# Kernel tuning notes

Measured on AMD Instinct MI355X. Metric: run time of the kernel, lower is better.

## Reference

```python
import jax, jax.numpy as jnp
import numpy as np

N_TOTAL = 204800  # total valid nodes across the batch
B = 1024          # number of graphs
D = 512           # input_dim (dim_node)
H = 512           # hidden width of NonLinearClassifier
C = 52            # num_classes
EPS = 1e-5        # BatchNorm eps


def setup_inputs() -> dict:
    key = jax.random.key(0)
    kz, k1, k2, k3 = jax.random.split(key, 4)
    # ragged per-graph node counts summing exactly to N_TOTAL
    rng = np.random.default_rng(0)
    counts = rng.integers(50, 350, size=B).astype(np.float64)
    counts = np.floor(counts * N_TOTAL / counts.sum()).astype(np.int64)
    counts[-1] += N_TOTAL - counts.sum()
    assert counts.min() > 0 and counts.sum() == N_TOTAL
    return {
        "z": jax.random.normal(kz, (N_TOTAL, D), dtype=jnp.float32),
        "batch_num_nodes": jnp.asarray(counts, dtype=jnp.int64),
        "w1": jax.random.normal(k1, (D, H), dtype=jnp.float32) * 0.02,
        "b1": jnp.zeros((H,), jnp.float32),
        "g1": jnp.ones((H,), jnp.float32),
        "beta1": jnp.zeros((H,), jnp.float32),
        "w2": jax.random.normal(k2, (H, H), dtype=jnp.float32) * 0.02,
        "b2": jnp.zeros((H,), jnp.float32),
        "g2": jnp.ones((H,), jnp.float32),
        "beta2": jnp.zeros((H,), jnp.float32),
        "w3": jax.random.normal(k3, (H, C), dtype=jnp.float32) * 0.02,
        "b3": jnp.zeros((C,), jnp.float32),
    }


def _batchnorm(x, gamma, beta):
    # training-mode BatchNorm1d: batch statistics (biased variance)
    m = x.mean(axis=0)
    v = x.var(axis=0)
    return gamma * (x - m) * jax.lax.rsqrt(v + EPS) + beta


def reference(z, batch_num_nodes, w1, b1, g1, beta1, w2, b2, g2, beta2, w3, b3):
    # fused segment-mean pooling (replaces torch.split + per-graph .mean loop)
    seg_ids = jnp.repeat(jnp.arange(B), batch_num_nodes, total_repeat_length=N_TOTAL)
    sums = jax.ops.segment_sum(z, seg_ids, num_segments=B)          # [B, D]
    graph_feats = sums / batch_num_nodes.astype(z.dtype)[:, None]   # [B, D]
    # NonLinearClassifier MLP (dropout inactive in eval / deterministic ref)
    h = jax.nn.relu(_batchnorm(graph_feats @ w1 + b1, g1, beta1))
    h = jax.nn.relu(_batchnorm(h @ w2 + b2, g2, beta2))
    return h @ w3 + b3  # [B, C] logits
```

## Files before the change

### kernel.cpp

```cpp
#include <hip/hip_runtime.h>

#define N_TOTAL 204800
#define NB 1024
#define DIM 512
#define NC 52
#define BN_EPS 1e-5f

typedef float nf4 __attribute__((ext_vector_type(4)));

__device__ inline float bn_relu1(float v, int f,
                                 const float* __restrict__ s1, const float* __restrict__ s2,
                                 const float* __restrict__ g, const float* __restrict__ beta) {
    float m  = s1[f] * (1.0f / NB);
    float vv = s2[f] * (1.0f / NB) - m * m;
    float is = rsqrtf(vv + BN_EPS);
    float h  = g[f] * (v - m) * is + beta[f];
    return h > 0.f ? h : 0.f;
}

__global__ __launch_bounds__(256) void k_pool(const float* __restrict__ z,
                                              const int* __restrict__ bnn,
                                              float* __restrict__ stats,
                                              float* __restrict__ X) {
    __shared__ nf4 buf[3][32];
    __shared__ int redA[4], redB[4];
    int g   = blockIdx.x;
    int cc  = blockIdx.y;
    int tid = threadIdx.x;
    int lane = tid & 63;
    int w    = tid >> 6;

    int t_all = 0;
#pragma unroll
    for (int k = 0; k < 4; k++) t_all += bnn[tid + k * 256];
#pragma unroll
    for (int s = 1; s < 64; s <<= 1) t_all += __shfl_xor(t_all, s);
    if (lane == 0) redA[w] = t_all;
    __syncthreads();
    bool is64 = (redA[0] + redA[1] + redA[2] + redA[3]) != N_TOTAL;

    int t_pre = 0;
#pragma unroll
    for (int k = 0; k < 4; k++) {
        int j = tid + k * 256;
        if (j < g) t_pre += is64 ? bnn[2 * j] : bnn[j];
    }
#pragma unroll
    for (int s = 1; s < 64; s <<= 1) t_pre += __shfl_xor(t_pre, s);
    if (lane == 0) redB[w] = t_pre;
    if (cc == 0 && g < 8) stats[g * 256 + tid] = 0.0f;
    __syncthreads();
    int s0 = redB[0] + redB[1] + redB[2] + redB[3];
    int n  = is64 ? bnn[2 * g] : bnn[g];
    float r = 1.0f / (float)n;

    int c4 = tid & 31;
    int rp = tid >> 5;
    const nf4* p = (const nf4*)z + (size_t)s0 * 128 + cc * 32 + c4;
    nf4 a0 = {0,0,0,0}, a1 = {0,0,0,0}, a2 = {0,0,0,0}, a3 = {0,0,0,0};
    int i = rp;
    for (; i + 56 < n; i += 64) {
        nf4 v0 = __builtin_nontemporal_load(&p[(size_t)(i +  0) * 128]);
        nf4 v1 = __builtin_nontemporal_load(&p[(size_t)(i +  8) * 128]);
        nf4 v2 = __builtin_nontemporal_load(&p[(size_t)(i + 16) * 128]);
        nf4 v3 = __builtin_nontemporal_load(&p[(size_t)(i + 24) * 128]);
        nf4 v4 = __builtin_nontemporal_load(&p[(size_t)(i + 32) * 128]);
        nf4 v5 = __builtin_nontemporal_load(&p[(size_t)(i + 40) * 128]);
        nf4 v6 = __builtin_nontemporal_load(&p[(size_t)(i + 48) * 128]);
        nf4 v7 = __builtin_nontemporal_load(&p[(size_t)(i + 56) * 128]);
        a0 += v0; a1 += v1; a2 += v2; a3 += v3;
        a0 += v4; a1 += v5; a2 += v6; a3 += v7;
    }
    for (; i < n; i += 8) {
        a0 += __builtin_nontemporal_load(&p[(size_t)i * 128]);
    }
    a0 += a1; a2 += a3; a0 += a2;
    a0.x += __shfl_xor(a0.x, 32); a0.y += __shfl_xor(a0.y, 32);
    a0.z += __shfl_xor(a0.z, 32); a0.w += __shfl_xor(a0.w, 32);
    if (w > 0 && lane < 32) buf[w - 1][c4] = a0;
    __syncthreads();
    if (w == 0 && lane < 32) {
        a0 += buf[0][c4]; a0 += buf[1][c4]; a0 += buf[2][c4];
        a0 *= r;
        ((nf4*)X)[(size_t)g * 128 + cc * 32 + c4] = a0;
    }
}

template <bool BNA>
__global__ __launch_bounds__(512) void k_gemm32x64(const float* __restrict__ A,
                                                   const float* __restrict__ W,
                                                   const float* __restrict__ bias,
                                                   const float* __restrict__ ps1,
                                                   const float* __restrict__ ps2,
                                                   const float* __restrict__ gam,
                                                   const float* __restrict__ bet,
                                                   float* __restrict__ Y,
                                                   float* __restrict__ os1,
                                                   float* __restrict__ os2) {
    __shared__ float As[32][34];
    __shared__ float Ws[32][68];
    int tid = threadIdx.x;
    int tx = tid & 31, ty = tid >> 5;
    int gr0 = blockIdx.x * 32;
    int gc0 = blockIdx.y * 64;

    int arow = (tid & 255) >> 3;
    int akq  = tid & 7;
    int wk  = tid >> 4;
    int wcq = tid & 15;

    float acc[2][2] = {};

    float4 ra = {0, 0, 0, 0};
    if (tid < 256) ra = *(const float4*)&A[(size_t)(gr0 + arow) * DIM + akq * 4];
    float4 rw = *(const float4*)&W[(size_t)wk * DIM + gc0 + wcq * 4];

    for (int kt = 0; kt < 16; kt++) {
        if (tid < 256) {
            float4 v = ra;
            if (BNA) {
                int f0 = kt * 32 + akq * 4;
                v.x = bn_relu1(v.x, f0 + 0, ps1, ps2, gam, bet);
                v.y = bn_relu1(v.y, f0 + 1, ps1, ps2, gam, bet);
                v.z = bn_relu1(v.z, f0 + 2, ps1, ps2, gam, bet);
                v.w = bn_relu1(v.w, f0 + 3, ps1, ps2, gam, bet);
            }
            As[akq * 4 + 0][arow] = v.x;
            As[akq * 4 + 1][arow] = v.y;
            As[akq * 4 + 2][arow] = v.z;
            As[akq * 4 + 3][arow] = v.w;
        }
        *(float4*)&Ws[wk][wcq * 4] = rw;
        __syncthreads();

        if (kt < 15) {
            int k0 = (kt + 1) * 32;
            if (tid < 256)
                ra = *(const float4*)&A[(size_t)(gr0 + arow) * DIM + k0 + akq * 4];
            rw = *(const float4*)&W[(size_t)(k0 + wk) * DIM + gc0 + wcq * 4];
        }

#pragma unroll
        for (int k = 0; k < 32; k++) {
            float2 a = *(const float2*)&As[k][ty * 2];
            float2 w = *(const float2*)&Ws[k][tx * 2];
            acc[0][0] += a.x * w.x; acc[0][1] += a.x * w.y;
            acc[1][0] += a.y * w.x; acc[1][1] += a.y * w.y;
        }
        __syncthreads();
    }

    float2 b = *(const float2*)&bias[gc0 + tx * 2];
    float s0 = 0, s1 = 0, q0 = 0, q1 = 0;
#pragma unroll
    for (int i = 0; i < 2; i++) {
        float2 y;
        y.x = acc[i][0] + b.x;
        y.y = acc[i][1] + b.y;
        *(float2*)&Y[(size_t)(gr0 + ty * 2 + i) * DIM + gc0 + tx * 2] = y;
        s0 += y.x; q0 += y.x * y.x;
        s1 += y.y; q1 += y.y * y.y;
    }
    s0 += __shfl_xor(s0, 32); q0 += __shfl_xor(q0, 32);
    s1 += __shfl_xor(s1, 32); q1 += __shfl_xor(q1, 32);
    if ((tid & 63) < 32) {
        atomicAdd(&os1[gc0 + tx * 2 + 0], s0);
        atomicAdd(&os1[gc0 + tx * 2 + 1], s1);
        atomicAdd(&os2[gc0 + tx * 2 + 0], q0);
        atomicAdd(&os2[gc0 + tx * 2 + 1], q1);
    }
}

__global__ __launch_bounds__(256) void k_gemm3(const float* __restrict__ Y2,
                                               const float* __restrict__ W,
                                               const float* __restrict__ bias,
                                               const float* __restrict__ s1,
                                               const float* __restrict__ s2,
                                               const float* __restrict__ gam,
                                               const float* __restrict__ bet,
                                               float* __restrict__ out) {
    __shared__ float As[4][DIM];
    int tid = threadIdx.x;
    int r0 = blockIdx.x * 4;
#pragma unroll
    for (int it = 0; it < 2; it++) {
        int idx = it * 256 + tid;
        int row = idx >> 7;
        int cq  = idx & 127;
        int f   = cq * 4;
        float4 v = *(const float4*)&Y2[(size_t)(r0 + row) * DIM + f];
        v.x = bn_relu1(v.x, f + 0, s1, s2, gam, bet);
        v.y = bn_relu1(v.y, f + 1, s1, s2, gam, bet);
        v.z = bn_relu1(v.z, f + 2, s1, s2, gam, bet);
        v.w = bn_relu1(v.w, f + 3, s1, s2, gam, bet);
        *(float4*)&As[row][f] = v;
    }
    __syncthreads();
    int col = tid & 63;
    int row = tid >> 6;
    if (col < NC) {
        float acc = 0.f;
#pragma unroll 8
        for (int k = 0; k < DIM; k += 4) {
            float4 a = *(const float4*)&As[row][k];
            acc += a.x * W[(size_t)(k + 0) * NC + col];
            acc += a.y * W[(size_t)(k + 1) * NC + col];
            acc += a.z * W[(size_t)(k + 2) * NC + col];
            acc += a.w * W[(size_t)(k + 3) * NC + col];
        }
        out[(size_t)(r0 + row) * NC + col] = acc + bias[col];
    }
}

extern "C" void kernel_launch(void* const* d_in, const int* in_sizes, int n_in,
                              void* d_out, int out_size, void* d_ws, size_t ws_size,
                              hipStream_t stream) {
    const float* z   = (const float*)d_in[0];
    const int*   bnn = (const int*)d_in[1];
    const float* w1  = (const float*)d_in[2];
    const float* b1  = (const float*)d_in[3];
    const float* g1  = (const float*)d_in[4];
    const float* be1 = (const float*)d_in[5];
    const float* w2  = (const float*)d_in[6];
    const float* b2  = (const float*)d_in[7];
    const float* g2  = (const float*)d_in[8];
    const float* be2 = (const float*)d_in[9];
    const float* w3  = (const float*)d_in[10];
    const float* b3  = (const float*)d_in[11];

    float* stats = (float*)d_ws;
    float* X     = stats + 2048;
    float* Y1    = X  + (size_t)NB * DIM;
    float* Y2    = Y1 + (size_t)NB * DIM;
    float* out   = (float*)d_out;

    k_pool<<<dim3(NB, 4), 256, 0, stream>>>(z, bnn, stats, X);

    dim3 gg(NB / 32, DIM / 64);
    k_gemm32x64<false><<<gg, 512, 0, stream>>>(X, w1, b1,
                                               nullptr, nullptr, nullptr, nullptr,
                                               Y1, stats, stats + 512);
    k_gemm32x64<true><<<gg, 512, 0, stream>>>(Y1, w2, b2,
                                              stats, stats + 512, g1, be1,
                                              Y2, stats + 1024, stats + 1536);
    k_gemm3<<<NB / 4, 256, 0, stream>>>(Y2, w3, b3,
                                        stats + 1024, stats + 1536, g2, be2, out);
}
```

Baseline: 619.9 us.

## Fuse three MLP GEMM kernels into one persistent kernel with grid barriers

Replaces the two GEMM launches and the final classifier launch with a single 256-block kernel that runs all three stages in sequence, separated by a software grid barrier built on atomic counters. Each block now computes a 32x64 tile with 256 threads doing 2x4 outputs apiece, replacing 512 threads doing 2x2. The goal is to remove kernel-launch gaps and tail effects between the small MLP stages. The cost is barrier spin overhead, and correctness depends on all 256 blocks being resident at the same time.

```diff
diff --git a/kernel.cpp b/kernel.cpp
--- a/kernel.cpp
+++ b/kernel.cpp
@@ -21,6 +21,7 @@
 __global__ __launch_bounds__(256) void k_pool(const float* __restrict__ z,
                                               const int* __restrict__ bnn,
                                               float* __restrict__ stats,
+                                              unsigned* __restrict__ bar,
                                               float* __restrict__ X) {
     __shared__ nf4 buf[3][32];
     __shared__ int redA[4], redB[4];
@@ -49,6 +50,7 @@
     for (int s = 1; s < 64; s <<= 1) t_pre += __shfl_xor(t_pre, s);
     if (lane == 0) redB[w] = t_pre;
     if (cc == 0 && g < 8) stats[g * 256 + tid] = 0.0f;
+    if (cc == 0 && g == 8 && tid < 4) bar[tid] = 0u;
     __syncthreads();
     int s0 = redB[0] + redB[1] + redB[2] + redB[3];
     int n  = is64 ? bnn[2 * g] : bnn[g];
@@ -86,102 +88,149 @@
     }
 }
 
+
+__device__ inline void grid_barrier(unsigned* cnt, unsigned* gen) {
+    __threadfence();
+    __syncthreads();
+    if (threadIdx.x == 0) {
+        unsigned g = atomicAdd(gen, 0u);
+        unsigned old = atomicAdd(cnt, 1u);
+        if (old == 255u) {
+            atomicExch(cnt, 0u);
+            atomicAdd(gen, 1u);
+        } else {
+            while (atomicAdd(gen, 0u) == g) { }
+        }
+    }
+    __syncthreads();
+    __threadfence();
+}
+
 template <bool BNA>
-__global__ __launch_bounds__(512) void k_gemm32x64(const float* __restrict__ A,
-                                                   const float* __restrict__ W,
-                                                   const float* __restrict__ bias,
-                                                   const float* __restrict__ ps1,
-                                                   const float* __restrict__ ps2,
-                                                   const float* __restrict__ gam,
-                                                   const float* __restrict__ bet,
-                                                   float* __restrict__ Y,
-                                                   float* __restrict__ os1,
-                                                   float* __restrict__ os2) {
+__device__ void gemm_phase(const float* __restrict__ A,
+                           const float* __restrict__ W,
+                           const float* __restrict__ bias,
+                           const float* __restrict__ ps1,
+                           const float* __restrict__ ps2,
+                           const float* __restrict__ gam,
+                           const float* __restrict__ bet,
+                           float* __restrict__ Y,
+                           float* __restrict__ os1,
+                           float* __restrict__ os2,
+                           float (&As)[32][34], float (&Ws)[32][68]) {
+    int tid = threadIdx.x;
+    int tx = tid & 15, ty = tid >> 4;
+    int gr0 = (blockIdx.x >> 3) * 32;
+    int gc0 = (blockIdx.x & 7) * 64;
+
+    int arow = tid >> 3;
+    int akq  = tid & 7;
+    int wk0 = tid >> 4;
+    int wcq = tid & 15;
+
+    float acc[2][4] = {};
+
+    float4 ra  = *(const float4*)&A[(size_t)(gr0 + arow) * DIM + akq * 4];
+    float4 rw0 = *(const float4*)&W[(size_t)wk0 * DIM + gc0 + wcq * 4];
+    float4 rw1 = *(const float4*)&W[(size_t)(wk0 + 16) * DIM + gc0 + wcq * 4];
+
+    for (int kt = 0; kt < 16; kt++) {
+        float4 v = ra;
+        if (BNA) {
+            int f0 = kt * 32 + akq * 4;
+            v.x = bn_relu1(v.x, f0 + 0, ps1, ps2, gam, bet);
+            v.y = bn_relu1(v.y, f0 + 1, ps1, ps2, gam, bet);
+            v.z = bn_relu1(v.z, f0 + 2, ps1, ps2, gam, bet);
+            v.w = bn_relu1(v.w, f0 + 3, ps1, ps2, gam, bet);
+        }
+        As[akq * 4 + 0][arow] = v.x;
+        As[akq * 4 + 1][arow] = v.y;
+        As[akq * 4 + 2][arow] = v.z;
+        As[akq * 4 + 3][arow] = v.w;
+        *(float4*)&Ws[wk0][wcq * 4]      = rw0;
+        *(float4*)&Ws[wk0 + 16][wcq * 4] = rw1;
+        __syncthreads();
+
+        if (kt < 15) {
+            int k0 = (kt + 1) * 32;
+            ra  = *(const float4*)&A[(size_t)(gr0 + arow) * DIM + k0 + akq * 4];
+            rw0 = *(const float4*)&W[(size_t)(k0 + wk0) * DIM + gc0 + wcq * 4];
+            rw1 = *(const float4*)&W[(size_t)(k0 + wk0 + 16) * DIM + gc0 + wcq * 4];
+        }
+
+#pragma unroll
+        for (int k = 0; k < 32; k++) {
+            float2 a = *(const float2*)&As[k][ty * 2];
+            float4 w = *(const float4*)&Ws[k][tx * 4];
+            acc[0][0] += a.x * w.x; acc[0][1] += a.x * w.y;
+            acc[0][2] += a.x * w.z; acc[0][3] += a.x * w.w;
+            acc[1][0] += a.y * w.x; acc[1][1] += a.y * w.y;
+            acc[1][2] += a.y * w.z; acc[1][3] += a.y * w.w;
+        }
+        __syncthreads();
+    }
+
+    float4 b = *(const float4*)&bias[gc0 + tx * 4];
+    float s[4] = {}, q[4] = {};
+#pragma unroll
+    for (int i = 0; i < 2; i++) {
+        float4 y;
+        y.x = acc[i][0] + b.x;
+        y.y = acc[i][1] + b.y;
+        y.z = acc[i][2] + b.z;
+        y.w = acc[i][3] + b.w;
+        *(float4*)&Y[(size_t)(gr0 + ty * 2 + i) * DIM + gc0 + tx * 4] = y;
+        s[0] += y.x; q[0] += y.x * y.x;
+        s[1] += y.y; q[1] += y.y * y.y;
+        s[2] += y.z; q[2] += y.z * y.z;
+        s[3] += y.w; q[3] += y.w * y.w;
+    }
+#pragma unroll
+    for (int j = 0; j < 4; j++) {
+        s[j] += __shfl_xor(s[j], 16); s[j] += __shfl_xor(s[j], 32);
+        q[j] += __shfl_xor(q[j], 16); q[j] += __shfl_xor(q[j], 32);
+    }
+    if ((ty & 3) == 0) {
+#pragma unroll
+        for (int j = 0; j < 4; j++) {
+            atomicAdd(&os1[gc0 + tx * 4 + j], s[j]);
+            atomicAdd(&os2[gc0 + tx * 4 + j], q[j]);
+        }
+    }
+}
+
+__global__ __launch_bounds__(256) void k_mlp(const float* __restrict__ X,
+                                             const float* __restrict__ w1,
+                                             const float* __restrict__ b1,
+                                             const float* __restrict__ g1,
+                                             const float* __restrict__ be1,
+                                             const float* __restrict__ w2,
+                                             const float* __restrict__ b2,
+                                             const float* __restrict__ g2,
+                                             const float* __restrict__ be2,
+                                             const float* __restrict__ w3,
+                                             const float* __restrict__ b3,
+                                             float* __restrict__ stats,
+                                             unsigned* __restrict__ bar,
+                                             float* __restrict__ Y1,
+                                             float* __restrict__ Y2,
+                                             float* __restrict__ out) {
     __shared__ float As[32][34];
     __shared__ float Ws[32][68];
-    int tid = threadIdx.x;
-    int tx = tid & 31, ty = tid >> 5;
-    int gr0 = blockIdx.x * 32;
-    int gc0 = blockIdx.y * 64;
-
-    int arow = (tid & 255) >> 3;
-    int akq  = tid & 7;
-    int wk  = tid >> 4;
-    int wcq = tid & 15;
-
-    float acc[2][2] = {};
-
-    float4 ra = {0, 0, 0, 0};
-    if (tid < 256) ra = *(const float4*)&A[(size_t)(gr0 + arow) * DIM + akq * 4];
-    float4 rw = *(const float4*)&W[(size_t)wk * DIM + gc0 + wcq * 4];
-
-    for (int kt = 0; kt < 16; kt++) {
-        if (tid < 256) {
-            float4 v = ra;
-            if (BNA) {
-                int f0 = kt * 32 + akq * 4;
-                v.x = bn_relu1(v.x, f0 + 0, ps1, ps2, gam, bet);
-                v.y = bn_relu1(v.y, f0 + 1, ps1, ps2, gam, bet);
-                v.z = bn_relu1(v.z, f0 + 2, ps1, ps2, gam, bet);
-                v.w = bn_relu1(v.w, f0 + 3, ps1, ps2, gam, bet);
-            }
-            As[akq * 4 + 0][arow] = v.x;
-            As[akq * 4 + 1][arow] = v.y;
-            As[akq * 4 + 2][arow] = v.z;
-            As[akq * 4 + 3][arow] = v.w;
-        }
-        *(float4*)&Ws[wk][wcq * 4] = rw;
-        __syncthreads();
-
-        if (kt < 15) {
-            int k0 = (kt + 1) * 32;
-            if (tid < 256)
-                ra = *(const float4*)&A[(size_t)(gr0 + arow) * DIM + k0 + akq * 4];
-            rw = *(const float4*)&W[(size_t)(k0 + wk) * DIM + gc0 + wcq * 4];
-        }
-
-#pragma unroll
-        for (int k = 0; k < 32; k++) {
-            float2 a = *(const float2*)&As[k][ty * 2];
-            float2 w = *(const float2*)&Ws[k][tx * 2];
-            acc[0][0] += a.x * w.x; acc[0][1] += a.x * w.y;
-            acc[1][0] += a.y * w.x; acc[1][1] += a.y * w.y;
-        }
-        __syncthreads();
-    }
-
-    float2 b = *(const float2*)&bias[gc0 + tx * 2];
-    float s0 = 0, s1 = 0, q0 = 0, q1 = 0;
-#pragma unroll
-    for (int i = 0; i < 2; i++) {
-        float2 y;
-        y.x = acc[i][0] + b.x;
-        y.y = acc[i][1] + b.y;
-        *(float2*)&Y[(size_t)(gr0 + ty * 2 + i) * DIM + gc0 + tx * 2] = y;
-        s0 += y.x; q0 += y.x * y.x;
-        s1 += y.y; q1 += y.y * y.y;
-    }
-    s0 += __shfl_xor(s0, 32); q0 += __shfl_xor(q0, 32);
-    s1 += __shfl_xor(s1, 32); q1 += __shfl_xor(q1, 32);
-    if ((tid & 63) < 32) {
-        atomicAdd(&os1[gc0 + tx * 2 + 0], s0);
-        atomicAdd(&os1[gc0 + tx * 2 + 1], s1);
-        atomicAdd(&os2[gc0 + tx * 2 + 0], q0);
-        atomicAdd(&os2[gc0 + tx * 2 + 1], q1);
-    }
-}
-
-__global__ __launch_bounds__(256) void k_gemm3(const float* __restrict__ Y2,
-                                               const float* __restrict__ W,
-                                               const float* __restrict__ bias,
-                                               const float* __restrict__ s1,
-                                               const float* __restrict__ s2,
-                                               const float* __restrict__ gam,
-                                               const float* __restrict__ bet,
-                                               float* __restrict__ out) {
-    __shared__ float As[4][DIM];
+    __shared__ float A3[4][DIM];
+
+    gemm_phase<false>(X, w1, b1, nullptr, nullptr, nullptr, nullptr,
+                      Y1, stats, stats + 512, As, Ws);
+    grid_barrier(bar, bar + 1);
+
+    gemm_phase<true>(Y1, w2, b2, stats, stats + 512, g1, be1,
+                     Y2, stats + 1024, stats + 1536, As, Ws);
+    grid_barrier(bar, bar + 1);
+
     int tid = threadIdx.x;
     int r0 = blockIdx.x * 4;
+    const float* s1 = stats + 1024;
+    const float* s2 = stats + 1536;
 #pragma unroll
     for (int it = 0; it < 2; it++) {
         int idx = it * 256 + tid;
@@ -189,11 +238,11 @@
         int cq  = idx & 127;
         int f   = cq * 4;
         float4 v = *(const float4*)&Y2[(size_t)(r0 + row) * DIM + f];
-        v.x = bn_relu1(v.x, f + 0, s1, s2, gam, bet);
-        v.y = bn_relu1(v.y, f + 1, s1, s2, gam, bet);
-        v.z = bn_relu1(v.z, f + 2, s1, s2, gam, bet);
-        v.w = bn_relu1(v.w, f + 3, s1, s2, gam, bet);
-        *(float4*)&As[row][f] = v;
+        v.x = bn_relu1(v.x, f + 0, s1, s2, g2, be2);
+        v.y = bn_relu1(v.y, f + 1, s1, s2, g2, be2);
+        v.z = bn_relu1(v.z, f + 2, s1, s2, g2, be2);
+        v.w = bn_relu1(v.w, f + 3, s1, s2, g2, be2);
+        *(float4*)&A3[row][f] = v;
     }
     __syncthreads();
     int col = tid & 63;
@@ -202,13 +251,13 @@
         float acc = 0.f;
 #pragma unroll 8
         for (int k = 0; k < DIM; k += 4) {
-            float4 a = *(const float4*)&As[row][k];
-            acc += a.x * W[(size_t)(k + 0) * NC + col];
-            acc += a.y * W[(size_t)(k + 1) * NC + col];
-            acc += a.z * W[(size_t)(k + 2) * NC + col];
-            acc += a.w * W[(size_t)(k + 3) * NC + col];
-        }
-        out[(size_t)(r0 + row) * NC + col] = acc + bias[col];
+            float4 a = *(const float4*)&A3[row][k];
+            acc += a.x * w3[(size_t)(k + 0) * NC + col];
+            acc += a.y * w3[(size_t)(k + 1) * NC + col];
+            acc += a.z * w3[(size_t)(k + 2) * NC + col];
+            acc += a.w * w3[(size_t)(k + 3) * NC + col];
+        }
+        out[(size_t)(r0 + row) * NC + col] = acc + b3[col];
     }
 }
 
@@ -228,21 +277,15 @@
     const float* w3  = (const float*)d_in[10];
     const float* b3  = (const float*)d_in[11];
 
-    float* stats = (float*)d_ws;
-    float* X     = stats + 2048;
-    float* Y1    = X  + (size_t)NB * DIM;
-    float* Y2    = Y1 + (size_t)NB * DIM;
-    float* out   = (float*)d_out;
-
-    k_pool<<<dim3(NB, 4), 256, 0, stream>>>(z, bnn, stats, X);
-
-    dim3 gg(NB / 32, DIM / 64);
-    k_gemm32x64<false><<<gg, 512, 0, stream>>>(X, w1, b1,
-                                               nullptr, nullptr, nullptr, nullptr,
-                                               Y1, stats, stats + 512);
-    k_gemm32x64<true><<<gg, 512, 0, stream>>>(Y1, w2, b2,
-                                              stats, stats + 512, g1, be1,
-                                              Y2, stats + 1024, stats + 1536);
-    k_gemm3<<<NB / 4, 256, 0, stream>>>(Y2, w3, b3,
-                                        stats + 1024, stats + 1536, g2, be2, out);
-}
+    float*    stats = (float*)d_ws;
+    unsigned* bar   = (unsigned*)(stats + 2048);
+    float*    X     = stats + 2048 + 4;
+    float*    Y1    = X  + (size_t)NB * DIM;
+    float*    Y2    = Y1 + (size_t)NB * DIM;
+    float*    out   = (float*)d_out;
+
+    k_pool<<<dim3(NB, 4), 256, 0, stream>>>(z, bnn, stats, bar, X);
+
+    k_mlp<<<256, 256, 0, stream>>>(X, w1, b1, g1, be1, w2, b2, g2, be2,
+                                   w3, b3, stats, bar, Y1, Y2, out);
+}
```

Result: slower. 678.6 us (+9.5%).
